# Optimization experiments

Hardware: AMD Instinct MI355X
Metric: run time of the kernel (lower is better)

## Reference

```python
import jax, jax.numpy as jnp
import numpy as np

B, IN, OUT = 65536, 1024, 1024
NB, D, H, L = 16, 32, 64, 4      # n_bundles, bundle_dim, norm_mlp hidden, n_latent_layers
TOT = NB * D                      # total latent dim = 512 (also encoder/decoder hidden)


def setup_inputs() -> dict:
    key = jax.random.key(0)
    ks = jax.random.split(key, 20)
    rn = lambda k, shape, s=0.02: (jax.random.normal(k, shape, dtype=jnp.float32) * s)
    return {
        "x": jax.random.normal(ks[0], (B, IN), dtype=jnp.float32),
        # encoder: Linear(IN,TOT), Linear(TOT,TOT), Linear(TOT,TOT)
        "enc_w1": rn(ks[1], (TOT, IN)), "enc_b1": jnp.zeros((TOT,), jnp.float32),
        "enc_w2": rn(ks[2], (TOT, TOT)), "enc_b2": jnp.zeros((TOT,), jnp.float32),
        "enc_w3": rn(ks[3], (TOT, TOT)), "enc_b3": jnp.zeros((TOT,), jnp.float32),
        # per-latent-layer norm_mlp: Linear(NB,H)+b, Linear(H,H)+b, Linear(H,NB) no bias
        "mlp1_w": rn(ks[4], (L, H, NB)), "mlp1_b": jnp.zeros((L, H), jnp.float32),
        "mlp2_w": rn(ks[5], (L, H, H)),  "mlp2_b": jnp.zeros((L, H), jnp.float32),
        "mlp3_w": rn(ks[6], (L, NB, H)),
        # mixing_weights[i][j] has shape (d_i, d_j); homogeneous -> [L,NB,NB,D,D], init 0.01*randn
        "mix_w": rn(ks[7], (L, NB, NB, D, D), 0.01),
        "gate_bias": jnp.zeros((L, NB), jnp.float32),
        # decoder: Linear(TOT,TOT), Linear(TOT,TOT), Linear(TOT,OUT)
        "dec_w1": rn(ks[8], (TOT, TOT)), "dec_b1": jnp.zeros((TOT,), jnp.float32),
        "dec_w2": rn(ks[9], (TOT, TOT)), "dec_b2": jnp.zeros((TOT,), jnp.float32),
        "dec_w3": rn(ks[10], (OUT, TOT)), "dec_b3": jnp.zeros((OUT,), jnp.float32),
    }


def _gelu(v):
    return jax.nn.gelu(v, approximate=False)  # torch nn.GELU default (erf)


def _soft_equivariant(z, m1w, m1b, m2w, m2b, m3w, mw, gb):
    # z: [B, TOT] -> bundles [B, NB, D] (homogeneous dims, contiguous split == reshape)
    zb = z.reshape(z.shape[0], NB, D)
    norms = jnp.linalg.norm(zb, axis=-1) + 1e-8          # [B, NB]
    h = _gelu(norms @ m1w.T + m1b)                        # [B, H]
    h = _gelu(h @ m2w.T + m2b)                            # [B, H]
    scales = jax.nn.softplus(h @ m3w.T)                   # [B, NB]
    equi = zb * scales[:, :, None]                        # [B, NB, D]
    # mixed_i = sum_j F.linear(bundles[j], W[i][j]) = bundles[j] @ W[i][j].T
    mixed = jnp.einsum('bjd,ijed->bie', zb, mw)           # [B, NB, D]
    gates = jax.nn.sigmoid(gb)                            # [NB]
    combined = equi + gates[None, :, None] * mixed        # [B, NB, D]
    return z + combined.reshape(z.shape[0], TOT)          # residual


def reference(x, enc_w1, enc_b1, enc_w2, enc_b2, enc_w3, enc_b3,
              mlp1_w, mlp1_b, mlp2_w, mlp2_b, mlp3_w, mix_w, gate_bias,
              dec_w1, dec_b1, dec_w2, dec_b2, dec_w3, dec_b3):
    # encoder
    z = _gelu(x @ enc_w1.T + enc_b1)
    z = _gelu(z @ enc_w2.T + enc_b2)
    z = z @ enc_w3.T + enc_b3
    # latent dynamics: L SoftEquivariantLayers (fixed small loop over layers)
    for l in range(L):
        z = _soft_equivariant(z, mlp1_w[l], mlp1_b[l], mlp2_w[l], mlp2_b[l],
                              mlp3_w[l], mix_w[l], gate_bias[l])
    # decoder
    y = _gelu(z @ dec_w1.T + dec_b1)
    y = _gelu(y @ dec_w2.T + dec_b2)
    return y @ dec_w3.T + dec_b3
```

## Files before the change

kernel.cpp:

```cpp
#include <hip/hip_runtime.h>
#include <hip/hip_bf16.h>

typedef float f32x4 __attribute__((ext_vector_type(4)));
typedef __bf16 bf16x8 __attribute__((ext_vector_type(8)));
typedef unsigned short u16x8 __attribute__((ext_vector_type(8)));
typedef unsigned short u16;

__device__ __forceinline__ u16 f2bf(float f) {
  __bf16 h = (__bf16)f;
  return __builtin_bit_cast(u16, h);
}
__device__ __forceinline__ float bf2f(u16 s) {
  return __uint_as_float(((unsigned int)s) << 16);
}
__device__ __forceinline__ float gelu_f(float x) {
  return 0.5f * x * (1.0f + erff(x * 0.70710678118654752f));
}
__device__ __forceinline__ void gload_lds16(const void* g, void* l) {
  __builtin_amdgcn_global_load_lds((const __attribute__((address_space(1))) void*)g,
                                   (__attribute__((address_space(3))) void*)l, 16, 0, 0);
}
#define MFMA(a, b, c) __builtin_amdgcn_mfma_f32_16x16x32_bf16((a), (b), (c), 0, 0, 0)
#define BARRIER_PINNED() do { \
    __builtin_amdgcn_s_barrier(); \
    asm volatile("" ::: "memory"); \
    __builtin_amdgcn_sched_barrier(0); \
  } while (0)

__global__ void cvt_all(const float* __restrict__ e1, const float* __restrict__ e2,
                        const float* __restrict__ e3, const float* __restrict__ d1,
                        const float* __restrict__ d2, const float* __restrict__ d3,
                        const float* __restrict__ mx, u16* __restrict__ dst)
{
  int i = blockIdx.x * blockDim.x + threadIdx.x;
  int stride = gridDim.x * blockDim.x;
  for (; i < 3145728; i += stride) {
    float v;
    if (i < 524288)        v = e1[i];
    else if (i < 786432)   v = e2[i - 524288];
    else if (i < 1048576)  v = e3[i - 786432];
    else if (i < 1310720)  v = d1[i - 1048576];
    else if (i < 1572864)  v = d2[i - 1310720];
    else if (i < 2097152)  v = d3[i - 1572864];
    else {
      int j = i - 2097152;
      int l = j >> 18, rem = j & 262143;
      int o = rem >> 9, k = rem & 511;
      int bi = o >> 5, e = o & 31, jj = k >> 5, dd = k & 31;
      v = mx[(((l * 16 + bi) * 16 + jj) * 32 + e) * 32 + dd];
    }
    dst[i] = f2bf(v);
  }
}

__global__ void cvt_x(const float* __restrict__ s, u16* __restrict__ d) {
  int i = blockIdx.x * blockDim.x + threadIdx.x;
  int stride = gridDim.x * blockDim.x;
  for (; i < 8388608; i += stride) {
    float4 v0 = *(const float4*)(s + (size_t)i * 8);
    float4 v1 = *(const float4*)(s + (size_t)i * 8 + 4);
    u16x8 u;
    u[0] = f2bf(v0.x); u[1] = f2bf(v0.y); u[2] = f2bf(v0.z); u[3] = f2bf(v0.w);
    u[4] = f2bf(v1.x); u[5] = f2bf(v1.y); u[6] = f2bf(v1.z); u[7] = f2bf(v1.w);
    *(u16x8*)(d + (size_t)i * 8) = u;
  }
}

template<int EPI>
__global__ __launch_bounds__(512, 2)
void gemm_panel(const u16* __restrict__ A, const u16* __restrict__ Bw,
                const float* __restrict__ bias, void* __restrict__ Cp,
                const float* __restrict__ scales, const float* __restrict__ gateBias,
                int N)
{
  extern __shared__ char smem[];
  char* Apan = smem;

  const int tid = threadIdx.x;
  const int lane = tid & 63;
  const int wid = tid >> 6;
  const int m0 = blockIdx.x << 7;

  const int wr = wid >> 2;
  const int wc = wid & 3;
  const int r16 = lane & 15;
  const int kg = (lane >> 4) << 3;
  const int sw = (r16 & 7) << 4;

  #pragma unroll
  for (int it = 0; it < 16; ++it) {
    int c = ((it * 8 + wid) << 6) + lane;
    int row = c >> 6;
    int cb = (c & 63) << 4;
    const char* g = (const char*)(A + ((size_t)(m0 + row) << 9)) + (cb ^ ((row & 7) << 4));
    gload_lds16(g, Apan + ((it * 8 + wid) << 10));
  }
  #pragma unroll
  for (int it = 0; it < 2; ++it) {
    int c = ((it * 8 + wid) << 6) + lane;
    int row = c >> 3;
    int cb = (c & 7) << 4;
    const char* g = (const char*)(Bw + ((size_t)row << 9)) + (cb ^ ((row & 7) << 4));
    gload_lds16(g, smem + 131072 + ((it * 8 + wid) << 10));
  }

  const int nN = N >> 7;
  const int S = nN << 3;
  f32x4 acc[4][2] = {};

  for (int s = 0; s < S; ++s) {
    const int kt = s & 7;
    const int nt = s >> 3;

    asm volatile("s_waitcnt vmcnt(0)" ::: "memory");
    BARRIER_PINNED();

    if (s + 1 < S) {
      const int ktn = (s + 1) & 7;
      const int ntn = (s + 1) >> 3;
      char* dst = smem + 131072 + (((s + 1) & 1) << 14);
      #pragma unroll
      for (int it = 0; it < 2; ++it) {
        int c = ((it * 8 + wid) << 6) + lane;
        int row = c >> 3;
        int cb = (c & 7) << 4;
        const char* g = (const char*)(Bw + ((size_t)((ntn << 7) + row) << 9) + (ktn << 6))
                        + (cb ^ ((row & 7) << 4));
        gload_lds16(g, dst + ((it * 8 + wid) << 10));
      }
    }

    const char* Bc = smem + 131072 + ((s & 1) << 14);
    #pragma unroll
    for (int kk = 0; kk < 64; kk += 32) {
      const int kbA = ((kt << 7) + ((kk + kg) << 1)) ^ sw;
      const int kbB = ((kk + kg) << 1) ^ sw;
      bf16x8 av[4], bv[2];
      #pragma unroll
      for (int m = 0; m < 4; ++m)
        av[m] = *(const bf16x8*)(Apan + ((wr * 64 + m * 16 + r16) << 10) + kbA);
      #pragma unroll
      for (int n = 0; n < 2; ++n)
        bv[n] = *(const bf16x8*)(Bc + ((wc * 32 + n * 16 + r16) << 7) + kbB);
      __builtin_amdgcn_s_setprio(1);
      #pragma unroll
      for (int m = 0; m < 4; ++m)
        #pragma unroll
        for (int n = 0; n < 2; ++n)
          acc[m][n] = MFMA(av[m], bv[n], acc[m][n]);
      __builtin_amdgcn_s_setprio(0);
    }

    if (kt == 7) {
      const int colBase = (nt << 7) + wc * 32 + r16;
      const int rowOff = wr * 64 + ((lane >> 4) << 2);
      #pragma unroll
      for (int n = 0; n < 2; ++n) {
        const int col = colBase + n * 16;
        float bv_ = 0.f, gate = 0.f;
        if constexpr (EPI == 0 || EPI == 1 || EPI == 3) bv_ = bias[col];
        if constexpr (EPI == 2) gate = 1.f / (1.f + expf(-gateBias[col >> 5]));
        #pragma unroll
        for (int m = 0; m < 4; ++m) {
          #pragma unroll
          for (int r = 0; r < 4; ++r) {
            const int rloc = rowOff + m * 16 + r;
            const int row = m0 + rloc;
            float v = acc[m][n][r];
            if constexpr (EPI == 0) {
              ((u16*)Cp)[(size_t)row * N + col] = f2bf(gelu_f(v + bv_));
            } else if constexpr (EPI == 1) {
              ((u16*)Cp)[(size_t)row * N + col] = f2bf(v + bv_);
            } else if constexpr (EPI == 2) {
              float sc = scales[(size_t)row * 16 + (col >> 5)];
              float zo = bf2f(*(const u16*)(Apan + ((size_t)rloc << 10) + (((col << 1)) ^ ((rloc & 7) << 4))));
              ((u16*)Cp)[(size_t)row * N + col] = f2bf(zo * (1.f + sc) + gate * v);
            } else {
              ((float*)Cp)[(size_t)row * N + col] = v + bv_;
            }
          }
        }
      }
      #pragma unroll
      for (int m = 0; m < 4; ++m)
        #pragma unroll
        for (int n = 0; n < 2; ++n)
          acc[m][n] = f32x4{0.f, 0.f, 0.f, 0.f};
    }
  }
}

__device__ __forceinline__ void stage_AB(const u16* __restrict__ Ab,
                                         const u16* __restrict__ Bb, int K,
                                         u16* At, u16* Bt, int wid, int lane)
{
  #pragma unroll
  for (int it = 0; it < 4; ++it) {
    int c = ((it * 4 + wid) << 6) + lane;
    int row = c >> 3;
    int cb = (c & 7) << 4;
    const char* g = (const char*)(Ab + (size_t)row * K) + (cb ^ ((row & 7) << 4));
    gload_lds16(g, (char*)At + ((it * 4 + wid) << 10));
  }
  #pragma unroll
  for (int it = 0; it < 2; ++it) {
    int c = ((it * 4 + wid) << 6) + lane;
    int row = c >> 3;
    int cb = (c & 7) << 4;
    const char* g = (const char*)(Bb + (size_t)row * K) + (cb ^ ((row & 7) << 4));
    gload_lds16(g, (char*)Bt + ((it * 4 + wid) << 10));
  }
}

__global__ __launch_bounds__(256, 2)
void gemm_p0(const u16* __restrict__ A, const u16* __restrict__ Bw,
             const float* __restrict__ bias, u16* __restrict__ Cp, int M, int N, int K)
{
  __shared__ u16 At[3][128 * 64];
  __shared__ u16 Bt[3][64 * 64];
  const int tid = threadIdx.x;
  const int lane = tid & 63;
  const int wid = tid >> 6;

  const int nx = N >> 6;
  const int ny = M >> 7;
  const int d = blockIdx.x;
  const int xcd = d & 7;
  const int seq = d >> 3;
  const int by = xcd * (ny >> 3) + seq / nx;
  const int bx = seq - (seq / nx) * nx;
  const int m0 = by << 7;
  const int n0 = bx << 6;

  const int wr = wid >> 1, wc = wid & 1;
  const int r16 = lane & 15;
  const int kg = (lane >> 4) << 3;
  const int sw = (r16 & 7) << 4;

  const u16* Ab = A + (size_t)m0 * K;
  const u16* Bb = Bw + (size_t)n0 * K;
  const int NT = K >> 6;

  f32x4 acc[4][2] = {};

  stage_AB(Ab,      Bb,      K, At[0], Bt[0], wid, lane);
  stage_AB(Ab + 64, Bb + 64, K, At[1], Bt[1], wid, lane);

  int cb = 0, ib = 2;
  for (int kt = 0; kt < NT; ++kt) {
    if (kt + 1 < NT) { asm volatile("s_waitcnt vmcnt(6)" ::: "memory"); }
    else             { asm volatile("s_waitcnt vmcnt(0)" ::: "memory"); }
    BARRIER_PINNED();

    if (kt + 2 < NT) {
      stage_AB(Ab + ((kt + 2) << 6), Bb + ((kt + 2) << 6), K, At[ib], Bt[ib], wid, lane);
      ib = (ib == 2) ? 0 : ib + 1;
    }

    const char* Ac = (const char*)At[cb];
    const char* Bc = (const char*)Bt[cb];
    #pragma unroll
    for (int kk = 0; kk < 64; kk += 32) {
      const int kb = ((kk + kg) << 1) ^ sw;
      bf16x8 av[4], bv[2];
      #pragma unroll
      for (int m = 0; m < 4; ++m)
        av[m] = *(const bf16x8*)(Ac + (wr * 64 + m * 16 + r16) * 128 + kb);
      #pragma unroll
      for (int n = 0; n < 2; ++n)
        bv[n] = *(const bf16x8*)(Bc + (wc * 32 + n * 16 + r16) * 128 + kb);
      __builtin_amdgcn_s_setprio(1);
      #pragma unroll
      for (int m = 0; m < 4; ++m)
        #pragma unroll
        for (int n = 0; n < 2; ++n)
          acc[m][n] = MFMA(av[m], bv[n], acc[m][n]);
      __builtin_amdgcn_s_setprio(0);
    }
    cb = (cb == 2) ? 0 : cb + 1;
  }

  const int colBase = n0 + wc * 32 + r16;
  const int rowBase = m0 + wr * 64 + ((lane >> 4) << 2);
  #pragma unroll
  for (int n = 0; n < 2; ++n) {
    int col = colBase + n * 16;
    float bv_ = bias[col];
    #pragma unroll
    for (int m = 0; m < 4; ++m)
      #pragma unroll
      for (int r = 0; r < 4; ++r) {
        int row = rowBase + m * 16 + r;
        Cp[(size_t)row * N + col] = f2bf(gelu_f(acc[m][n][r] + bv_));
      }
  }
}

__global__ __launch_bounds__(256, 2)
void norm_mlp2(const u16* __restrict__ z,
               const float* __restrict__ w1, const float* __restrict__ b1,
               const float* __restrict__ w2, const float* __restrict__ b2,
               const float* __restrict__ w3, float* __restrict__ scales)
{
  __shared__ float nrm[256][17];
  const int tid = threadIdx.x;
  const size_t base = (size_t)blockIdx.x << 8;

  #pragma unroll
  for (int p = 0; p < 16; ++p) {
    const int C = (p << 8) + tid;
    const int r = C >> 4, b = C & 15;
    const u16* zp = z + ((base + r) << 9) + (b << 5);
    float ss = 0.f;
    #pragma unroll
    for (int q = 0; q < 4; ++q) {
      u16x8 v = *(const u16x8*)(zp + q * 8);
      #pragma unroll
      for (int j = 0; j < 8; ++j) { float f = bf2f(v[j]); ss += f * f; }
    }
    nrm[r][b] = sqrtf(ss) + 1e-8f;
  }
  __syncthreads();

  float nr[16];
  #pragma unroll
  for (int i = 0; i < 16; ++i) nr[i] = nrm[tid][i];

  float h2[64];
  #pragma unroll
  for (int j = 0; j < 64; ++j) h2[j] = b2[j];

  for (int kt = 0; kt < 4; ++kt) {
    float h1t[16];
    #pragma unroll
    for (int k16 = 0; k16 < 16; ++k16) {
      const int k = (kt << 4) + k16;
      float t = b1[k];
      #pragma unroll
      for (int i = 0; i < 16; ++i) t += nr[i] * w1[k * 16 + i];
      h1t[k16] = gelu_f(t);
    }
    const float* w2t = w2 + (kt << 4);
    #pragma unroll
    for (int j = 0; j < 64; ++j) {
      float s = 0.f;
      #pragma unroll
      for (int k16 = 0; k16 < 16; ++k16) s += h1t[k16] * w2t[j * 64 + k16];
      h2[j] += s;
    }
  }
  #pragma unroll
  for (int j = 0; j < 64; ++j) h2[j] = gelu_f(h2[j]);

  float* srow = scales + ((base + tid) << 4);
  #pragma unroll
  for (int b = 0; b < 16; ++b) {
    float s = 0.f;
    #pragma unroll
    for (int k = 0; k < 64; ++k) s += h2[k] * w3[b * 64 + k];
    s = (s > 20.f) ? s : log1pf(expf(s));
    srow[b] = s;
  }
}

#define PANEL_SMEM 163840

extern "C" void kernel_launch(void* const* d_in, const int* in_sizes, int n_in,
                              void* d_out, int out_size, void* d_ws, size_t ws_size,
                              hipStream_t stream)
{
  (void)in_sizes; (void)n_in; (void)out_size; (void)ws_size;
  const float* x      = (const float*)d_in[0];
  const float* enc_w1 = (const float*)d_in[1];
  const float* enc_b1 = (const float*)d_in[2];
  const float* enc_w2 = (const float*)d_in[3];
  const float* enc_b2 = (const float*)d_in[4];
  const float* enc_w3 = (const float*)d_in[5];
  const float* enc_b3 = (const float*)d_in[6];
  const float* mlp1_w = (const float*)d_in[7];
  const float* mlp1_b = (const float*)d_in[8];
  const float* mlp2_w = (const float*)d_in[9];
  const float* mlp2_b = (const float*)d_in[10];
  const float* mlp3_w = (const float*)d_in[11];
  const float* mix_w  = (const float*)d_in[12];
  const float* gate_b = (const float*)d_in[13];
  const float* dec_w1 = (const float*)d_in[14];
  const float* dec_b1 = (const float*)d_in[15];
  const float* dec_w2 = (const float*)d_in[16];
  const float* dec_b2 = (const float*)d_in[17];
  const float* dec_w3 = (const float*)d_in[18];
  const float* dec_b3 = (const float*)d_in[19];

  char* ws = (char*)d_ws;
  const int M = 65536;

  u16*   xb     = (u16*)ws;
  u16*   zA     = (u16*)(ws + 134217728ULL);
  u16*   zB     = (u16*)ws;
  float* scales = (float*)(ws + 201326592ULL);
  u16*   wBase  = (u16*)(ws + 205520896ULL);
  u16* wE1 = wBase;
  u16* wE2 = wE1 + 524288;
  u16* wE3 = wE2 + 262144;
  u16* wD1 = wE3 + 262144;
  u16* wD2 = wD1 + 262144;
  u16* wD3 = wD2 + 262144;
  u16* wMix = wD3 + 524288;

  hipError_t e;
  e = hipFuncSetAttribute(reinterpret_cast<const void*>(&gemm_panel<0>),
                          hipFuncAttributeMaxDynamicSharedMemorySize, PANEL_SMEM);
  e = hipFuncSetAttribute(reinterpret_cast<const void*>(&gemm_panel<1>),
                          hipFuncAttributeMaxDynamicSharedMemorySize, PANEL_SMEM);
  e = hipFuncSetAttribute(reinterpret_cast<const void*>(&gemm_panel<2>),
                          hipFuncAttributeMaxDynamicSharedMemorySize, PANEL_SMEM);
  e = hipFuncSetAttribute(reinterpret_cast<const void*>(&gemm_panel<3>),
                          hipFuncAttributeMaxDynamicSharedMemorySize, PANEL_SMEM);
  (void)e;

  cvt_all<<<512, 256, 0, stream>>>(enc_w1, enc_w2, enc_w3, dec_w1, dec_w2, dec_w3,
                                   mix_w, wBase);

  dim3 pblk(512);
  const int pgrid = 512;

  cvt_x<<<2048, 256, 0, stream>>>(x, xb);
  gemm_p0<<<8 * 512, dim3(256), 0, stream>>>(xb, wE1, enc_b1, zA, M, 512, 1024);
  gemm_panel<0><<<pgrid, pblk, PANEL_SMEM, stream>>>(zA, wE2, enc_b2, zB, nullptr, nullptr, 512);
  gemm_panel<1><<<pgrid, pblk, PANEL_SMEM, stream>>>(zB, wE3, enc_b3, zA, nullptr, nullptr, 512);

  u16* cur = zA;
  u16* nxt = zB;
  for (int l = 0; l < 4; ++l) {
    norm_mlp2<<<256, dim3(256), 0, stream>>>(cur, mlp1_w + l * 1024, mlp1_b + l * 64,
                                             mlp2_w + l * 4096, mlp2_b + l * 64,
                                             mlp3_w + l * 1024, scales);
    gemm_panel<2><<<pgrid, pblk, PANEL_SMEM, stream>>>(cur, wMix + (size_t)l * 262144,
                                                       nullptr, nxt, scales, gate_b + l * 16, 512);
    u16* t = cur; cur = nxt; nxt = t;
  }

  gemm_panel<0><<<pgrid, pblk, PANEL_SMEM, stream>>>(cur, wD1, dec_b1, nxt, nullptr, nullptr, 512);
  { u16* t = cur; cur = nxt; nxt = t; }
  gemm_panel<0><<<pgrid, pblk, PANEL_SMEM, stream>>>(cur, wD2, dec_b2, nxt, nullptr, nullptr, 512);
  { u16* t = cur; cur = nxt; nxt = t; }
  gemm_panel<3><<<pgrid, pblk, PANEL_SMEM, stream>>>(cur, wD3, dec_b3, d_out, nullptr, nullptr, 1024);
}
```

Before: 1.388 ms.

## Replace panel GEMMs with wide 64x512 tile GEMM streaming both A and B

Replaces the A-panel-resident GEMM (128 rows held in LDS, looping over N tiles) and the separate first-layer GEMM with a single kernel. Each block computes a 64-row by 512-column tile, streaming 64-wide K slices of A and B through double-buffered LDS, and each of 8 waves owns 64 columns. The residual input for the mixing layer is now read from global memory instead of LDS, and the 1024-wide output layer is split into two launches over column halves. The aim is better reuse per staged A byte and fewer B reloads, at the cost of re-reading the whole weight matrix per 64 rows, using 4x4 accumulators per wave, and doing more global traffic in the epilogue.

```diff
diff --git a/kernel.cpp b/kernel.cpp
--- a/kernel.cpp
+++ b/kernel.cpp
@@ -68,231 +68,103 @@
 
 template<int EPI>
 __global__ __launch_bounds__(512, 2)
-void gemm_panel(const u16* __restrict__ A, const u16* __restrict__ Bw,
-                const float* __restrict__ bias, void* __restrict__ Cp,
-                const float* __restrict__ scales, const float* __restrict__ gateBias,
-                int N)
+void gemm_wide(const u16* __restrict__ A, const u16* __restrict__ Bw,
+               const float* __restrict__ bias, void* __restrict__ Cp,
+               const u16* __restrict__ zOld, const float* __restrict__ scales,
+               const float* __restrict__ gateBias, int N, int nOff, int K)
 {
   extern __shared__ char smem[];
-  char* Apan = smem;
-
   const int tid = threadIdx.x;
   const int lane = tid & 63;
   const int wid = tid >> 6;
-  const int m0 = blockIdx.x << 7;
-
-  const int wr = wid >> 2;
-  const int wc = wid & 3;
+  const int m0 = blockIdx.x << 6;
+
   const int r16 = lane & 15;
   const int kg = (lane >> 4) << 3;
   const int sw = (r16 & 7) << 4;
 
-  #pragma unroll
-  for (int it = 0; it < 16; ++it) {
-    int c = ((it * 8 + wid) << 6) + lane;
-    int row = c >> 6;
-    int cb = (c & 63) << 4;
-    const char* g = (const char*)(A + ((size_t)(m0 + row) << 9)) + (cb ^ ((row & 7) << 4));
-    gload_lds16(g, Apan + ((it * 8 + wid) << 10));
-  }
-  #pragma unroll
-  for (int it = 0; it < 2; ++it) {
-    int c = ((it * 8 + wid) << 6) + lane;
-    int row = c >> 3;
-    int cb = (c & 7) << 4;
-    const char* g = (const char*)(Bw + ((size_t)row << 9)) + (cb ^ ((row & 7) << 4));
-    gload_lds16(g, smem + 131072 + ((it * 8 + wid) << 10));
-  }
-
-  const int nN = N >> 7;
-  const int S = nN << 3;
-  f32x4 acc[4][2] = {};
-
-  for (int s = 0; s < S; ++s) {
-    const int kt = s & 7;
-    const int nt = s >> 3;
-
+  const int NT = K >> 6;
+  f32x4 acc[4][4] = {};
+
+  auto stage = [&](int kt, int b) {
+    {
+      int c = tid;
+      int row = c >> 3;
+      int cb = (c & 7) << 4;
+      const char* g = (const char*)(A + (size_t)(m0 + row) * K + (kt << 6))
+                      + (cb ^ ((row & 7) << 4));
+      gload_lds16(g, smem + (b << 13) + (wid << 10));
+    }
+    #pragma unroll
+    for (int p = 0; p < 8; ++p) {
+      int c = (p << 9) + tid;
+      int row = c >> 3;
+      int cb = (c & 7) << 4;
+      const char* g = (const char*)(Bw + (size_t)(nOff + row) * K + (kt << 6))
+                      + (cb ^ ((row & 7) << 4));
+      gload_lds16(g, smem + 16384 + (b << 16) + (((p << 3) + wid) << 10));
+    }
+  };
+
+  stage(0, 0);
+  asm volatile("s_waitcnt vmcnt(0)" ::: "memory");
+  BARRIER_PINNED();
+
+  for (int kt = 0; kt < NT; ++kt) {
+    const int cur = kt & 1;
+    if (kt + 1 < NT) stage(kt + 1, cur ^ 1);
+
+    const char* Ac = smem + (cur << 13);
+    const char* Bc = smem + 16384 + (cur << 16);
+    #pragma unroll
+    for (int kk = 0; kk < 64; kk += 32) {
+      const int kb = ((kk + kg) << 1) ^ sw;
+      bf16x8 av[4], bv[4];
+      #pragma unroll
+      for (int m = 0; m < 4; ++m)
+        av[m] = *(const bf16x8*)(Ac + (m * 16 + r16) * 128 + kb);
+      #pragma unroll
+      for (int n = 0; n < 4; ++n)
+        bv[n] = *(const bf16x8*)(Bc + ((wid << 6) + n * 16 + r16) * 128 + kb);
+      __builtin_amdgcn_s_setprio(1);
+      #pragma unroll
+      for (int m = 0; m < 4; ++m)
+        #pragma unroll
+        for (int n = 0; n < 4; ++n)
+          acc[m][n] = MFMA(av[m], bv[n], acc[m][n]);
+      __builtin_amdgcn_s_setprio(0);
+    }
     asm volatile("s_waitcnt vmcnt(0)" ::: "memory");
     BARRIER_PINNED();
-
-    if (s + 1 < S) {
-      const int ktn = (s + 1) & 7;
-      const int ntn = (s + 1) >> 3;
-      char* dst = smem + 131072 + (((s + 1) & 1) << 14);
-      #pragma unroll
-      for (int it = 0; it < 2; ++it) {
-        int c = ((it * 8 + wid) << 6) + lane;
-        int row = c >> 3;
-        int cb = (c & 7) << 4;
-        const char* g = (const char*)(Bw + ((size_t)((ntn << 7) + row) << 9) + (ktn << 6))
-                        + (cb ^ ((row & 7) << 4));
-        gload_lds16(g, dst + ((it * 8 + wid) << 10));
-      }
-    }
-
-    const char* Bc = smem + 131072 + ((s & 1) << 14);
-    #pragma unroll
-    for (int kk = 0; kk < 64; kk += 32) {
-      const int kbA = ((kt << 7) + ((kk + kg) << 1)) ^ sw;
-      const int kbB = ((kk + kg) << 1) ^ sw;
-      bf16x8 av[4], bv[2];
-      #pragma unroll
-      for (int m = 0; m < 4; ++m)
-        av[m] = *(const bf16x8*)(Apan + ((wr * 64 + m * 16 + r16) << 10) + kbA);
-      #pragma unroll
-      for (int n = 0; n < 2; ++n)
-        bv[n] = *(const bf16x8*)(Bc + ((wc * 32 + n * 16 + r16) << 7) + kbB);
-      __builtin_amdgcn_s_setprio(1);
-      #pragma unroll
-      for (int m = 0; m < 4; ++m)
-        #pragma unroll
-        for (int n = 0; n < 2; ++n)
-          acc[m][n] = MFMA(av[m], bv[n], acc[m][n]);
-      __builtin_amdgcn_s_setprio(0);
-    }
-
-    if (kt == 7) {
-      const int colBase = (nt << 7) + wc * 32 + r16;
-      const int rowOff = wr * 64 + ((lane >> 4) << 2);
-      #pragma unroll
-      for (int n = 0; n < 2; ++n) {
-        const int col = colBase + n * 16;
-        float bv_ = 0.f, gate = 0.f;
-        if constexpr (EPI == 0 || EPI == 1 || EPI == 3) bv_ = bias[col];
-        if constexpr (EPI == 2) gate = 1.f / (1.f + expf(-gateBias[col >> 5]));
-        #pragma unroll
-        for (int m = 0; m < 4; ++m) {
-          #pragma unroll
-          for (int r = 0; r < 4; ++r) {
-            const int rloc = rowOff + m * 16 + r;
-            const int row = m0 + rloc;
-            float v = acc[m][n][r];
-            if constexpr (EPI == 0) {
-              ((u16*)Cp)[(size_t)row * N + col] = f2bf(gelu_f(v + bv_));
-            } else if constexpr (EPI == 1) {
-              ((u16*)Cp)[(size_t)row * N + col] = f2bf(v + bv_);
-            } else if constexpr (EPI == 2) {
-              float sc = scales[(size_t)row * 16 + (col >> 5)];
-              float zo = bf2f(*(const u16*)(Apan + ((size_t)rloc << 10) + (((col << 1)) ^ ((rloc & 7) << 4))));
-              ((u16*)Cp)[(size_t)row * N + col] = f2bf(zo * (1.f + sc) + gate * v);
-            } else {
-              ((float*)Cp)[(size_t)row * N + col] = v + bv_;
-            }
-          }
+  }
+
+  const int colBase = nOff + (wid << 6) + r16;
+  const int rowBase = m0 + ((lane >> 4) << 2);
+  #pragma unroll
+  for (int n = 0; n < 4; ++n) {
+    const int col = colBase + n * 16;
+    float bv_ = 0.f, gate = 0.f;
+    if constexpr (EPI == 0 || EPI == 1 || EPI == 3) bv_ = bias[col];
+    if constexpr (EPI == 2) gate = 1.f / (1.f + expf(-gateBias[(col - nOff) >> 5]));
+    #pragma unroll
+    for (int m = 0; m < 4; ++m) {
+      #pragma unroll
+      for (int r = 0; r < 4; ++r) {
+        const int row = rowBase + m * 16 + r;
+        float v = acc[m][n][r];
+        if constexpr (EPI == 0) {
+          ((u16*)Cp)[(size_t)row * N + col] = f2bf(gelu_f(v + bv_));
+        } else if constexpr (EPI == 1) {
+          ((u16*)Cp)[(size_t)row * N + col] = f2bf(v + bv_);
+        } else if constexpr (EPI == 2) {
+          float sc = scales[(size_t)row * 16 + ((col - nOff) >> 5)];
+          float zo = bf2f(zOld[(size_t)row * 512 + (col - nOff)]);
+          ((u16*)Cp)[(size_t)row * N + col] = f2bf(zo * (1.f + sc) + gate * v);
+        } else {
+          ((float*)Cp)[(size_t)row * N + col] = v + bv_;
         }
       }
-      #pragma unroll
-      for (int m = 0; m < 4; ++m)
-        #pragma unroll
-        for (int n = 0; n < 2; ++n)
-          acc[m][n] = f32x4{0.f, 0.f, 0.f, 0.f};
-    }
-  }
-}
-
-__device__ __forceinline__ void stage_AB(const u16* __restrict__ Ab,
-                                         const u16* __restrict__ Bb, int K,
-                                         u16* At, u16* Bt, int wid, int lane)
-{
-  #pragma unroll
-  for (int it = 0; it < 4; ++it) {
-    int c = ((it * 4 + wid) << 6) + lane;
-    int row = c >> 3;
-    int cb = (c & 7) << 4;
-    const char* g = (const char*)(Ab + (size_t)row * K) + (cb ^ ((row & 7) << 4));
-    gload_lds16(g, (char*)At + ((it * 4 + wid) << 10));
-  }
-  #pragma unroll
-  for (int it = 0; it < 2; ++it) {
-    int c = ((it * 4 + wid) << 6) + lane;
-    int row = c >> 3;
-    int cb = (c & 7) << 4;
-    const char* g = (const char*)(Bb + (size_t)row * K) + (cb ^ ((row & 7) << 4));
-    gload_lds16(g, (char*)Bt + ((it * 4 + wid) << 10));
-  }
-}
-
-__global__ __launch_bounds__(256, 2)
-void gemm_p0(const u16* __restrict__ A, const u16* __restrict__ Bw,
-             const float* __restrict__ bias, u16* __restrict__ Cp, int M, int N, int K)
-{
-  __shared__ u16 At[3][128 * 64];
-  __shared__ u16 Bt[3][64 * 64];
-  const int tid = threadIdx.x;
-  const int lane = tid & 63;
-  const int wid = tid >> 6;
-
-  const int nx = N >> 6;
-  const int ny = M >> 7;
-  const int d = blockIdx.x;
-  const int xcd = d & 7;
-  const int seq = d >> 3;
-  const int by = xcd * (ny >> 3) + seq / nx;
-  const int bx = seq - (seq / nx) * nx;
-  const int m0 = by << 7;
-  const int n0 = bx << 6;
-
-  const int wr = wid >> 1, wc = wid & 1;
-  const int r16 = lane & 15;
-  const int kg = (lane >> 4) << 3;
-  const int sw = (r16 & 7) << 4;
-
-  const u16* Ab = A + (size_t)m0 * K;
-  const u16* Bb = Bw + (size_t)n0 * K;
-  const int NT = K >> 6;
-
-  f32x4 acc[4][2] = {};
-
-  stage_AB(Ab,      Bb,      K, At[0], Bt[0], wid, lane);
-  stage_AB(Ab + 64, Bb + 64, K, At[1], Bt[1], wid, lane);
-
-  int cb = 0, ib = 2;
-  for (int kt = 0; kt < NT; ++kt) {
-    if (kt + 1 < NT) { asm volatile("s_waitcnt vmcnt(6)" ::: "memory"); }
-    else             { asm volatile("s_waitcnt vmcnt(0)" ::: "memory"); }
-    BARRIER_PINNED();
-
-    if (kt + 2 < NT) {
-      stage_AB(Ab + ((kt + 2) << 6), Bb + ((kt + 2) << 6), K, At[ib], Bt[ib], wid, lane);
-      ib = (ib == 2) ? 0 : ib + 1;
-    }
-
-    const char* Ac = (const char*)At[cb];
-    const char* Bc = (const char*)Bt[cb];
-    #pragma unroll
-    for (int kk = 0; kk < 64; kk += 32) {
-      const int kb = ((kk + kg) << 1) ^ sw;
-      bf16x8 av[4], bv[2];
-      #pragma unroll
-      for (int m = 0; m < 4; ++m)
-        av[m] = *(const bf16x8*)(Ac + (wr * 64 + m * 16 + r16) * 128 + kb);
-      #pragma unroll
-      for (int n = 0; n < 2; ++n)
-        bv[n] = *(const bf16x8*)(Bc + (wc * 32 + n * 16 + r16) * 128 + kb);
-      __builtin_amdgcn_s_setprio(1);
-      #pragma unroll
-      for (int m = 0; m < 4; ++m)
-        #pragma unroll
-        for (int n = 0; n < 2; ++n)
-          acc[m][n] = MFMA(av[m], bv[n], acc[m][n]);
-      __builtin_amdgcn_s_setprio(0);
-    }
-    cb = (cb == 2) ? 0 : cb + 1;
-  }
-
-  const int colBase = n0 + wc * 32 + r16;
-  const int rowBase = m0 + wr * 64 + ((lane >> 4) << 2);
-  #pragma unroll
-  for (int n = 0; n < 2; ++n) {
-    int col = colBase + n * 16;
-    float bv_ = bias[col];
-    #pragma unroll
-    for (int m = 0; m < 4; ++m)
-      #pragma unroll
-      for (int r = 0; r < 4; ++r) {
-        int row = rowBase + m * 16 + r;
-        Cp[(size_t)row * N + col] = f2bf(gelu_f(acc[m][n][r] + bv_));
-      }
+    }
   }
 }
 
@@ -363,7 +235,7 @@
   }
 }
 
-#define PANEL_SMEM 163840
+#define WIDE_SMEM 147456
 
 extern "C" void kernel_launch(void* const* d_in, const int* in_sizes, int n_in,
                               void* d_out, int out_size, void* d_ws, size_t ws_size,
@@ -408,26 +280,26 @@
   u16* wMix = wD3 + 524288;
 
   hipError_t e;
-  e = hipFuncSetAttribute(reinterpret_cast<const void*>(&gemm_panel<0>),
-                          hipFuncAttributeMaxDynamicSharedMemorySize, PANEL_SMEM);
-  e = hipFuncSetAttribute(reinterpret_cast<const void*>(&gemm_panel<1>),
-                          hipFuncAttributeMaxDynamicSharedMemorySize, PANEL_SMEM);
-  e = hipFuncSetAttribute(reinterpret_cast<const void*>(&gemm_panel<2>),
-                          hipFuncAttributeMaxDynamicSharedMemorySize, PANEL_SMEM);
-  e = hipFuncSetAttribute(reinterpret_cast<const void*>(&gemm_panel<3>),
-                          hipFuncAttributeMaxDynamicSharedMemorySize, PANEL_SMEM);
+  e = hipFuncSetAttribute(reinterpret_cast<const void*>(&gemm_wide<0>),
+                          hipFuncAttributeMaxDynamicSharedMemorySize, WIDE_SMEM);
+  e = hipFuncSetAttribute(reinterpret_cast<const void*>(&gemm_wide<1>),
+                          hipFuncAttributeMaxDynamicSharedMemorySize, WIDE_SMEM);
+  e = hipFuncSetAttribute(reinterpret_cast<const void*>(&gemm_wide<2>),
+                          hipFuncAttributeMaxDynamicSharedMemorySize, WIDE_SMEM);
+  e = hipFuncSetAttribute(reinterpret_cast<const void*>(&gemm_wide<3>),
+                          hipFuncAttributeMaxDynamicSharedMemorySize, WIDE_SMEM);
   (void)e;
 
   cvt_all<<<512, 256, 0, stream>>>(enc_w1, enc_w2, enc_w3, dec_w1, dec_w2, dec_w3,
                                    mix_w, wBase);
 
-  dim3 pblk(512);
-  const int pgrid = 512;
+  dim3 blk(512);
+  const int grid = 1024;
 
   cvt_x<<<2048, 256, 0, stream>>>(x, xb);
-  gemm_p0<<<8 * 512, dim3(256), 0, stream>>>(xb, wE1, enc_b1, zA, M, 512, 1024);
-  gemm_panel<0><<<pgrid, pblk, PANEL_SMEM, stream>>>(zA, wE2, enc_b2, zB, nullptr, nullptr, 512);
-  gemm_panel<1><<<pgrid, pblk, PANEL_SMEM, stream>>>(zB, wE3, enc_b3, zA, nullptr, nullptr, 512);
+  gemm_wide<0><<<grid, blk, WIDE_SMEM, stream>>>(xb, wE1, enc_b1, zA, nullptr, nullptr, nullptr, 512, 0, 1024);
+  gemm_wide<0><<<grid, blk, WIDE_SMEM, stream>>>(zA, wE2, enc_b2, zB, nullptr, nullptr, nullptr, 512, 0, 512);
+  gemm_wide<1><<<grid, blk, WIDE_SMEM, stream>>>(zB, wE3, enc_b3, zA, nullptr, nullptr, nullptr, 512, 0, 512);
 
   u16* cur = zA;
   u16* nxt = zB;
@@ -435,14 +307,15 @@
     norm_mlp2<<<256, dim3(256), 0, stream>>>(cur, mlp1_w + l * 1024, mlp1_b + l * 64,
                                              mlp2_w + l * 4096, mlp2_b + l * 64,
                                              mlp3_w + l * 1024, scales);
-    gemm_panel<2><<<pgrid, pblk, PANEL_SMEM, stream>>>(cur, wMix + (size_t)l * 262144,
-                                                       nullptr, nxt, scales, gate_b + l * 16, 512);
+    gemm_wide<2><<<grid, blk, WIDE_SMEM, stream>>>(cur, wMix + (size_t)l * 262144, nullptr, nxt,
+                                                   cur, scales, gate_b + l * 16, 512, 0, 512);
     u16* t = cur; cur = nxt; nxt = t;
   }
 
-  gemm_panel<0><<<pgrid, pblk, PANEL_SMEM, stream>>>(cur, wD1, dec_b1, nxt, nullptr, nullptr, 512);
+  gemm_wide<0><<<grid, blk, WIDE_SMEM, stream>>>(cur, wD1, dec_b1, nxt, nullptr, nullptr, nullptr, 512, 0, 512);
   { u16* t = cur; cur = nxt; nxt = t; }
-  gemm_panel<0><<<pgrid, pblk, PANEL_SMEM, stream>>>(cur, wD2, dec_b2, nxt, nullptr, nullptr, 512);
+  gemm_wide<0><<<grid, blk, WIDE_SMEM, stream>>>(cur, wD2, dec_b2, nxt, nullptr, nullptr, nullptr, 512, 0, 512);
   { u16* t = cur; cur = nxt; nxt = t; }
-  gemm_panel<3><<<pgrid, pblk, PANEL_SMEM, stream>>>(cur, wD3, dec_b3, d_out, nullptr, nullptr, 1024);
-}
+  gemm_wide<3><<<grid, blk, WIDE_SMEM, stream>>>(cur, wD3, dec_b3, d_out, nullptr, nullptr, nullptr, 1024, 0, 512);
+  gemm_wide<3><<<grid, blk, WIDE_SMEM, stream>>>(cur, wD3, dec_b3, d_out, nullptr, nullptr, nullptr, 1024, 512, 512);
+}
```

Result: no change. 1.403 ms (+1.1%).
